# Kernel tuning notes

Hardware: AMD Instinct MI355X
Metric: run time of the kernel (lower is better)

Reference implementation:

```python
import jax, jax.numpy as jnp
import numpy as np

N = 10000      # num nodes
DEG = 8        # avg out-degree
E = N * DEG    # num bonds (directed edges)
D_IN = 128; D_HID = 128; D_OUT = 128; H = 16; HD = D_OUT // H
NG = 20; G_STOP = 10.0   # GaussianSmearing: 20 gaussians on [0, 10]
NF = 3                   # AngularEncoding num_funcs -> 1 + 4*NF = 13 feats


def _triplets(row, col, n):
    # numpy replica of BondUpdateLayer.triplets (SparseTensor version):
    # for each edge e=(j=row[e] -> i=col[e]), enumerate edges e'=(k -> j), drop k==i.
    order = np.argsort(col, kind='stable')          # edges sorted by target node
    in_count = np.bincount(col, minlength=n)
    in_start = np.concatenate([np.zeros(1, np.int64), np.cumsum(in_count)])
    num_t = in_count[row]                           # triplets per edge e
    T = int(num_t.sum())
    idx_ji = np.repeat(np.arange(row.size), num_t)
    within = np.arange(T) - np.repeat(np.cumsum(num_t) - num_t, num_t)
    idx_kj = order[in_start[row[idx_ji]] + within]
    idx_k = row[idx_kj]
    idx_i = col[idx_ji]
    idx_j = row[idx_ji]
    mask = idx_i != idx_k
    return idx_i[mask], idx_j[mask], idx_k[mask], idx_kj[mask], idx_ji[mask]


def setup_inputs() -> dict:
    key = jax.random.key(0)
    ks = jax.random.split(key, 8)
    rng = np.random.default_rng(0)
    src = np.repeat(np.arange(N), DEG)
    dst = (src + rng.integers(1, N, size=E)) % N    # random targets, never self-loop
    i_i, i_j, i_k, i_kj, i_ji = _triplets(src, dst, N)
    kv_dim = D_IN + 2 * NG + (1 + 4 * NF)           # 128 + 40 + 13 = 181

    def mlp_params(k, din):
        k1, k2 = jax.random.split(k)
        return {
            'W1': jax.random.normal(k1, (din, D_HID)) * 0.05, 'b1': jnp.zeros(D_HID),
            'g': jnp.ones(D_HID), 'b': jnp.zeros(D_HID),
            'W2': jax.random.normal(k2, (D_HID, D_OUT)) * 0.05, 'b2': jnp.zeros(D_OUT),
        }

    inp = {
        'h': jax.random.normal(ks[3], (N, D_IN)),
        'h_bond': jax.random.normal(ks[4], (E, D_IN)),
        'pos': jax.random.normal(ks[5], (N, 3)) * 3.0,
    }
    for name, k, din in (('hk', ks[0], kv_dim), ('hv', ks[1], kv_dim), ('hq', ks[2], D_IN)):
        for pn, v in mlp_params(k, din).items():
            inp[f'{name}_{pn}'] = v
    inp['bond_row'] = jnp.asarray(src, jnp.int32)
    inp['bond_col'] = jnp.asarray(dst, jnp.int32)
    inp['idx_i'] = jnp.asarray(i_i, jnp.int32)
    inp['idx_j'] = jnp.asarray(i_j, jnp.int32)
    inp['idx_k'] = jnp.asarray(i_k, jnp.int32)
    inp['idx_kj'] = jnp.asarray(i_kj, jnp.int32)
    inp['idx_ji'] = jnp.asarray(i_ji, jnp.int32)
    return inp


def _gauss(d):
    off = jnp.linspace(0.0, G_STOP, NG)
    coeff = -0.5 / (off[1] - off[0]) ** 2
    return jnp.exp(coeff * (d[:, None] - off) ** 2)


def _ang(a):
    freqs = jnp.asarray([1.0, 2.0, 3.0, 1.0, 0.5, 1.0 / 3.0])   # [i+1] + [1/(i+1)]
    x = a[:, None] * freqs
    return jnp.concatenate([a[:, None], jnp.sin(x), jnp.cos(x)], -1)


def _mlp(x, W1, b1, g, b, W2, b2):
    # Linear -> LayerNorm -> ReLU -> Linear
    hdn = x @ W1 + b1
    mu = hdn.mean(-1, keepdims=True)
    var = ((hdn - mu) ** 2).mean(-1, keepdims=True)
    hdn = jax.nn.relu(g * (hdn - mu) * jax.lax.rsqrt(var + 1e-5) + b)
    return hdn @ W2 + b2


def _forward(h, h_bond, pos,
             hk_W1, hk_b1, hk_g, hk_b, hk_W2, hk_b2,
             hv_W1, hv_b1, hv_g, hv_b, hv_W2, hv_b2,
             hq_W1, hq_b1, hq_g, hq_b, hq_W2, hq_b2,
             bond_row, bond_col, idx_i, idx_j, idx_k, idx_kj, idx_ji):
    # per-edge distance features (i=col, j=row in the torch code)
    dist = jnp.linalg.norm(pos[bond_col] - pos[bond_row], axis=-1)   # [E]
    r_feat = _gauss(dist)                                            # [E, 20]
    # per-triplet angle features
    pi = pos[idx_i]
    pji = pos[idx_j] - pi
    pki = pos[idx_k] - pi
    a = (pji * pki).sum(-1)
    bcr = jnp.linalg.norm(jnp.cross(pji, pki), axis=-1)
    a_feat = _ang(jnp.arctan2(bcr, a))                               # [T, 13]
    kv = jnp.concatenate([h_bond[idx_kj], r_feat[idx_kj], r_feat[idx_ji], a_feat], -1)  # [T, 181]
    T = kv.shape[0]
    k = _mlp(kv, hk_W1, hk_b1, hk_g, hk_b, hk_W2, hk_b2).reshape(T, H, HD)
    v = _mlp(kv, hv_W1, hv_b1, hv_g, hv_b, hv_W2, hv_b2).reshape(T, H, HD)
    q = _mlp(h_bond[idx_ji], hq_W1, hq_b1, hq_g, hq_b, hq_W2, hq_b2).reshape(T, H, HD)
    logits = (q * k).sum(-1) / np.sqrt(HD)                           # [T, H]
    # scatter_softmax over idx_ji (segments = edges)
    mx = jax.ops.segment_max(logits, idx_ji, num_segments=E)
    ex = jnp.exp(logits - mx[idx_ji])
    den = jax.ops.segment_sum(ex, idx_ji, num_segments=E)
    alpha = ex / den[idx_ji]                                         # [T, H]
    out = jax.ops.segment_sum(alpha[:, :, None] * v, idx_ji, num_segments=E)  # [E, H, HD]
    return out.reshape(E, D_OUT)


def reference(h, h_bond, pos,
              hk_W1, hk_b1, hk_g, hk_b, hk_W2, hk_b2,
              hv_W1, hv_b1, hv_g, hv_b, hv_W2, hv_b2,
              hq_W1, hq_b1, hq_g, hq_b, hq_W2, hq_b2,
              bond_row, bond_col, idx_i, idx_j, idx_k, idx_kj, idx_ji):
    return _forward(h, h_bond, pos,
                    hk_W1, hk_b1, hk_g, hk_b, hk_W2, hk_b2,
                    hv_W1, hv_b1, hv_g, hv_b, hv_W2, hv_b2,
                    hq_W1, hq_b1, hq_g, hq_b, hq_W2, hq_b2,
                    bond_row, bond_col, idx_i, idx_j, idx_k, idx_kj, idx_ji)
```

## Files before the change

kernel.cpp:

```cpp
#include <hip/hip_runtime.h>
#include <hip/hip_bf16.h>
#include <math.h>

typedef __hip_bfloat16 bf16;
typedef unsigned int u32;

__device__ __forceinline__ float b2f(bf16 x){ return __bfloat162float(x); }
__device__ __forceinline__ bf16  f2b(float x){ return __float2bfloat16(x); }
__device__ __forceinline__ float lo16(u32 u){ return __uint_as_float(u << 16); }
__device__ __forceinline__ float hi16(u32 u){ return __uint_as_float(u & 0xFFFF0000u); }
__device__ __forceinline__ u32 bfbits(float x){
    u32 u = __float_as_uint(x);
    return (u + 0x7FFFu + ((u >> 16) & 1u)) >> 16;
}

#define RSQRT8 0.35355339059327373f
#define G_STEP (10.0f/19.0f)
#define G_COEF (-0.5f/(G_STEP*G_STEP))

__device__ __forceinline__ constexpr int PERM4(int h){
    return ((h&1)<<3) | ((h&2)<<1) | ((h&4)>>1) | ((h&8)>>3);
}

__device__ __forceinline__ float fast_atan2(float y, float x){
    float ax = fabsf(x);
    float mn = fminf(y, ax), mx = fmaxf(y, ax);
    float t = mn / fmaxf(mx, 1e-30f);
    float s = t*t;
    float p = t * (0.99997726f + s*(-0.33262347f + s*(0.19354346f +
              s*(-0.11643287f + s*(0.05265332f + s*(-0.01172120f))))));
    float r = (y > ax) ? (1.5707963267948966f - p) : p;
    r = (x < 0.f) ? (3.14159265358979323f - r) : r;
    return r;
}


__global__ void seg_start_kernel(const int* __restrict__ idx_ji, int T,
                                 int* __restrict__ seg, int E)
{
    int e = blockIdx.x * blockDim.x + threadIdx.x;
    if (e > E) return;
    int lo = 0, hi = T;
    while (lo < hi) { int mid = (lo + hi) >> 1; if (idx_ji[mid] < e) lo = mid + 1; else hi = mid; }
    seg[e] = lo;
}

__global__ void marker_kernel(float* out, int n){
    int i = blockIdx.x * blockDim.x + threadIdx.x;
    if (i < n) out[i] = 12345.0f;
}

__global__ void pack_w2(const float* __restrict__ Wk2, const float* __restrict__ Wv2,
                        u32* __restrict__ kw2t, u32* __restrict__ vw2t)
{
    int idx = blockIdx.x*256 + threadIdx.x;
    if (idx >= 8192) return;
    int c = idx >> 6, p = idx & 63;
    kw2t[idx] = bfbits(Wk2[(size_t)(2*p)*128 + c]) | (bfbits(Wk2[(size_t)(2*p+1)*128 + c]) << 16);
    int j = idx >> 7, o = idx & 127;
    vw2t[idx] = bfbits(Wv2[(size_t)(2*j)*128 + o]) | (bfbits(Wv2[(size_t)(2*j+1)*128 + o]) << 16);
}

__global__ __launch_bounds__(128) void q_kernel(
    const float* __restrict__ W1, const float* __restrict__ B1,
    const float* __restrict__ G,  const float* __restrict__ Bln,
    const float* __restrict__ W2, const float* __restrict__ B2,
    const float* __restrict__ h_bond, bf16* __restrict__ qout, int E)
{
    __shared__ u32 sW[128*65];
    __shared__ float sH[16][130];
    __shared__ float sX[4][130];
    __shared__ float sRed[4][4];
    int tid = threadIdx.x; int wv = tid>>6, lane = tid&63;
    int base = blockIdx.x * 16;

    for (int idx = tid; idx < 128*128; idx += 128) {
        int i = idx >> 7, d = idx & 127;
        ((bf16*)sW)[d*130 + i] = f2b(W1[idx]);
    }
    __syncthreads();
    for (int e4 = 0; e4 < 16; e4 += 4) {
        #pragma unroll
        for (int q = 0; q < 4; ++q) {
            int e = base + e4 + q;
            sX[q][tid] = (e < E) ? h_bond[(size_t)e*128 + tid] : 0.f;
        }
        __syncthreads();
        float b1t = B1[tid];
        float ac[4] = {b1t, b1t, b1t, b1t};
        const u32* wrow = &sW[tid*65];
        #pragma unroll 4
        for (int j = 0; j < 64; ++j) {
            u32 w = wrow[j]; float wl = lo16(w), wh = hi16(w);
            #pragma unroll
            for (int q = 0; q < 4; ++q)
                ac[q] += sX[q][2*j]*wl + sX[q][2*j+1]*wh;
        }
        float s1v[4], s2v[4];
        #pragma unroll
        for (int q = 0; q < 4; ++q) { s1v[q] = ac[q]; s2v[q] = ac[q]*ac[q]; }
        #pragma unroll
        for (int m = 1; m < 64; m <<= 1) {
            #pragma unroll
            for (int q = 0; q < 4; ++q) {
                s1v[q] += __shfl_xor(s1v[q], m, 64);
                s2v[q] += __shfl_xor(s2v[q], m, 64);
            }
        }
        if (lane == 0) {
            #pragma unroll
            for (int q = 0; q < 4; ++q) { sRed[q][wv*2] = s1v[q]; sRed[q][wv*2+1] = s2v[q]; }
        }
        __syncthreads();
        float gt = G[tid], bt = Bln[tid];
        #pragma unroll
        for (int q = 0; q < 4; ++q) {
            float tot = sRed[q][0] + sRed[q][2], tot2 = sRed[q][1] + sRed[q][3];
            float mu = tot * (1.f/128.f);
            float var = fmaxf(tot2 * (1.f/128.f) - mu*mu, 0.f);
            float nv = gt * (ac[q] - mu) * rsqrtf(var + 1e-5f) + bt;
            sH[e4+q][tid] = fmaxf(nv, 0.f);
        }
        __syncthreads();
    }
    for (int idx = tid; idx < 128*128; idx += 128) {
        int i = idx >> 7, d = idx & 127;
        ((bf16*)sW)[d*130 + i] = f2b(W2[idx]);
    }
    __syncthreads();
    for (int e4 = 0; e4 < 16; e4 += 4) {
        float b2t = B2[tid];
        float ac[4] = {b2t, b2t, b2t, b2t};
        const u32* wrow = &sW[tid*65];
        #pragma unroll 4
        for (int j = 0; j < 64; ++j) {
            u32 w = wrow[j]; float wl = lo16(w), wh = hi16(w);
            #pragma unroll
            for (int q = 0; q < 4; ++q)
                ac[q] += sH[e4+q][2*j]*wl + sH[e4+q][2*j+1]*wh;
        }
        #pragma unroll
        for (int q = 0; q < 4; ++q) {
            int e = base + e4 + q;
            if (e < E) qout[(size_t)e*128 + tid] = f2b(ac[q]);
        }
    }
}

__global__ __launch_bounds__(128) void p_prep(
    const float* __restrict__ W1, const float* __restrict__ h_bond,
    const float* __restrict__ pos, const int* __restrict__ row,
    const int* __restrict__ col, bf16* __restrict__ P1, int E)
{
    __shared__ u32 sW[128*75];
    __shared__ float sX[4][152];
    int tid = threadIdx.x;
    for (int idx = tid; idx < 148*128; idx += 128) {
        int i = idx >> 7, d = idx & 127;
        ((bf16*)sW)[d*150 + i] = f2b(W1[idx]);
    }
    __syncthreads();
    int base = blockIdx.x * 16;
    for (int e4 = 0; e4 < 16; e4 += 4) {
        #pragma unroll
        for (int q = 0; q < 4; ++q) {
            int e = base + e4 + q;
            sX[q][tid] = (e < E) ? h_bond[(size_t)e*128 + tid] : 0.f;
        }
        if (tid < 80) {
            int q = tid / 20, g = tid % 20;
            int e = base + e4 + q;
            float rf = 0.f;
            if (e < E) {
                int i0 = col[e], j0 = row[e];
                float dx = pos[(size_t)i0*3+0] - pos[(size_t)j0*3+0];
                float dy = pos[(size_t)i0*3+1] - pos[(size_t)j0*3+1];
                float dz = pos[(size_t)i0*3+2] - pos[(size_t)j0*3+2];
                float dist = sqrtf(dx*dx + dy*dy + dz*dz);
                float t = dist - (float)g * G_STEP;
                rf = __expf(G_COEF * t * t);
            }
            sX[q][128 + g] = rf;
        }
        __syncthreads();
        float acc0 = 0.f, acc1 = 0.f, acc2 = 0.f, acc3 = 0.f;
        const u32* wrow = &sW[tid*75];
        #pragma unroll 4
        for (int j = 0; j < 74; ++j) {
            u32 w = wrow[j]; float wl = lo16(w), wh = hi16(w);
            acc0 += sX[0][2*j]*wl + sX[0][2*j+1]*wh;
            acc1 += sX[1][2*j]*wl + sX[1][2*j+1]*wh;
            acc2 += sX[2][2*j]*wl + sX[2][2*j+1]*wh;
            acc3 += sX[3][2*j]*wl + sX[3][2*j+1]*wh;
        }
        int e = base + e4;
        if (e   < E) P1[(size_t)e*128     + tid] = f2b(acc0);
        if (e+1 < E) P1[(size_t)(e+1)*128 + tid] = f2b(acc1);
        if (e+2 < E) P1[(size_t)(e+2)*128 + tid] = f2b(acc2);
        if (e+3 < E) P1[(size_t)(e+3)*128 + tid] = f2b(acc3);
        __syncthreads();
    }
}

#define EDGE_P2(W1full, b1v_, P2a_, P2b_) \
    float P2a_ = b1v_.x, P2b_ = b1v_.y; \
    { const float2* wbp = (const float2*)((W1full) + (size_t)148*128); \
      for (int g2 = 0; g2 < 20; ++g2) { \
        float tg = dist - (float)g2 * G_STEP; \
        float rf = __expf(G_COEF * tg * tg); \
        float2 wb = wbp[g2*64 + lane]; \
        P2a_ += rf * wb.x; \
        P2b_ += rf * wb.y; \
      } }

#define GEOM(S) \
    float dt##S = ax*bx##S + ay*by##S + az*bz##S; \
    float cxx##S = ay*bz##S - az*by##S, cyy##S = az*bx##S - ax*bz##S, czz##S = ax*by##S - ay*bx##S; \
    float bb##S = cxx##S*cxx##S + cyy##S*cyy##S + czz##S*czz##S; \
    float bc##S = sqrtf(bb##S); \
    float ih##S = rsqrtf(fmaxf(dt##S*dt##S + bb##S, 1e-30f)); \
    float c1##S = dt##S * ih##S, s1##S = bc##S * ih##S; \
    float ang##S = fast_atan2(bc##S, dt##S); \
    float sh##S = sqrtf(fmaxf(0.5f*(1.f - c1##S), 0.f)); \
    float ch##S = sqrtf(fmaxf(0.5f*(1.f + c1##S), 0.f)); \
    float st3##S, ct3##S; __sincosf((1.f/3.f)*ang##S, &st3##S, &ct3##S);

#define FEAT(fidx, valX, valY) { \
    u32 wk_ = sWA[0][(fidx)*64 + lane]; \
    u32 wu_ = sWA[1][(fidx)*64 + lane]; \
    float wkl_ = lo16(wk_), wkh_ = hi16(wk_), wvl_ = lo16(wu_), wvh_ = hi16(wu_); \
    float fx_ = (valX), fy_ = (valY); \
    v0kX += fx_*wkl_; v1kX += fx_*wkh_; v0vX += fx_*wvl_; v1vX += fx_*wvh_; \
    v0kY += fy_*wkl_; v1kY += fy_*wkh_; v0vY += fy_*wvl_; v1vY += fy_*wvh_; }

#define LNSTATS(v0_, v1_, TOT, TOT2) { \
    float sum_ = (v0_) + (v1_), ssq_ = (v0_)*(v0_) + (v1_)*(v1_); \
    float r_ = ((lane&1) ? ssq_ : sum_) + __shfl_xor((lane&1) ? sum_ : ssq_, 1, 64); \
    r_ += __shfl_xor(r_, 2, 64);  r_ += __shfl_xor(r_, 4, 64); \
    r_ += __shfl_xor(r_, 8, 64);  r_ += __shfl_xor(r_, 16, 64); \
    r_ += __shfl_xor(r_, 32, 64); \
    float o_ = __shfl_xor(r_, 1, 64); \
    TOT = (lane&1) ? o_ : r_;  TOT2 = (lane&1) ? r_ : o_; }

#define LNAPPLY(TOT, TOT2, v0_, v1_, g_, b_, H0, H1) { \
    float mu_ = (TOT) * (1.f/128.f); \
    float var_ = fmaxf((TOT2) * (1.f/128.f) - mu_*mu_, 0.f); \
    float rs_ = rsqrtf(var_ + 1e-5f); \
    H0 = fmaxf(g_.x*((v0_)-mu_)*rs_ + b_.x, 0.f); \
    H1 = fmaxf(g_.y*((v1_)-mu_)*rs_ + b_.y, 0.f); }

#define BFLY(P, LG) { \
    float a8_[8]; \
    { int up_ = lane & 1; \
      _Pragma("unroll") \
      for (int i_ = 0; i_ < 8; ++i_) { \
        float kp_ = up_ ? P[i_+8] : P[i_]; \
        float sd_ = up_ ? P[i_]   : P[i_+8]; \
        a8_[i_] = kp_ + __shfl_xor(sd_, 1, 64); } } \
    float a4_[4]; \
    { int up_ = lane & 2; \
      _Pragma("unroll") \
      for (int i_ = 0; i_ < 4; ++i_) { \
        float kp_ = up_ ? a8_[i_+4] : a8_[i_]; \
        float sd_ = up_ ? a8_[i_]   : a8_[i_+4]; \
        a4_[i_] = kp_ + __shfl_xor(sd_, 2, 64); } } \
    float a2_[2]; \
    { int up_ = lane & 4; \
      _Pragma("unroll") \
      for (int i_ = 0; i_ < 2; ++i_) { \
        float kp_ = up_ ? a4_[i_+2] : a4_[i_]; \
        float sd_ = up_ ? a4_[i_]   : a4_[i_+2]; \
        a2_[i_] = kp_ + __shfl_xor(sd_, 4, 64); } } \
    float a1_; \
    { int up_ = lane & 8; \
      float kp_ = up_ ? a2_[1] : a2_[0]; \
      float sd_ = up_ ? a2_[0] : a2_[1]; \
      a1_ = kp_ + __shfl_xor(sd_, 8, 64); } \
    a1_ += __shfl_xor(a1_, 16, 64); \
    a1_ += __shfl_xor(a1_, 32, 64); \
    LG = a1_ * RSQRT8; }

__global__ __launch_bounds__(256, 2)
void fused_kernel(
    const u32* __restrict__ kw2t, const u32* __restrict__ vw2t,
    const float* __restrict__ Wk1, const float* __restrict__ Bk1,
    const float* __restrict__ Gkg, const float* __restrict__ Bkln,
    const float* __restrict__ Wv1, const float* __restrict__ Bv1,
    const float* __restrict__ Gvg, const float* __restrict__ Bvln,
    const float* __restrict__ B2v,
    const bf16* __restrict__ qf, const bf16* __restrict__ P1k, const bf16* __restrict__ P1v,
    const float* __restrict__ pos, const int* __restrict__ seg,
    const int* __restrict__ idx_kj, const int* __restrict__ idx_k,
    const int* __restrict__ row, const int* __restrict__ col,
    float* __restrict__ out, int E)
{
    __shared__ u32 sS[4][16*66];
    __shared__ u32 sWA[2][11*64];
    __shared__ float2 sEx[4][16];
    int tid = threadIdx.x, lane = tid & 63, wv = tid >> 6;

    if (tid < 128) {
        int path = tid >> 6, l = tid & 63;
        const float* W1full = path ? Wv1 : Wk1;
        const float2* wap = (const float2*)(W1full + (size_t)168*128);
        float2 w0  = wap[ 0*64 + l];
        float2 w1  = wap[ 1*64 + l];
        float2 w2  = wap[ 2*64 + l];
        float2 w3  = wap[ 3*64 + l];
        float2 w4  = wap[ 4*64 + l];
        float2 w5  = wap[ 5*64 + l];
        float2 w6  = wap[ 6*64 + l];
        float2 w7  = wap[ 7*64 + l];
        float2 w8  = wap[ 8*64 + l];
        float2 w9  = wap[ 9*64 + l];
        float2 w10 = wap[10*64 + l];
        float2 w11 = wap[11*64 + l];
        float2 w12 = wap[12*64 + l];
        u32* dst = &sWA[path][0];
        dst[ 0*64 + l] = bfbits(w0.x)       | (bfbits(w0.y)       << 16);
        dst[ 1*64 + l] = bfbits(w1.x+w4.x)  | (bfbits(w1.y+w4.y)  << 16);
        dst[ 2*64 + l] = bfbits(w2.x)       | (bfbits(w2.y)       << 16);
        dst[ 3*64 + l] = bfbits(w3.x)       | (bfbits(w3.y)       << 16);
        dst[ 4*64 + l] = bfbits(w5.x)       | (bfbits(w5.y)       << 16);
        dst[ 5*64 + l] = bfbits(w6.x)       | (bfbits(w6.y)       << 16);
        dst[ 6*64 + l] = bfbits(w7.x+w10.x) | (bfbits(w7.y+w10.y) << 16);
        dst[ 7*64 + l] = bfbits(w8.x)       | (bfbits(w8.y)       << 16);
        dst[ 8*64 + l] = bfbits(w9.x)       | (bfbits(w9.y)       << 16);
        dst[ 9*64 + l] = bfbits(w11.x)      | (bfbits(w11.y)      << 16);
        dst[10*64 + l] = bfbits(w12.x)      | (bfbits(w12.y)      << 16);
    }
    __syncthreads();

    int e = __builtin_amdgcn_readfirstlane(blockIdx.x*4 + wv);
    if (e >= E) return;
    int s0 = __builtin_amdgcn_readfirstlane(seg[e]);
    int s1 = __builtin_amdgcn_readfirstlane(seg[e+1]);
    if (s1 <= s0) { out[(size_t)e*128 + lane] = 0.f; out[(size_t)e*128 + 64 + lane] = 0.f; return; }

    float2 b1k = ((const float2*)Bk1)[lane];
    float2 gk  = ((const float2*)Gkg)[lane];
    float2 bk  = ((const float2*)Bkln)[lane];
    float2 b1v = ((const float2*)Bv1)[lane];
    float2 gv  = ((const float2*)Gvg)[lane];
    float2 bv  = ((const float2*)Bvln)[lane];

    int i0 = __builtin_amdgcn_readfirstlane(col[e]);
    int j0 = __builtin_amdgcn_readfirstlane(row[e]);
    float pix = pos[(size_t)i0*3+0], piy = pos[(size_t)i0*3+1], piz = pos[(size_t)i0*3+2];
    float pjx = pos[(size_t)j0*3+0], pjy = pos[(size_t)j0*3+1], pjz = pos[(size_t)j0*3+2];
    float dxx = pix-pjx, dyy = piy-pjy, dzz = piz-pjz;
    float dist = sqrtf(dxx*dxx + dyy*dyy + dzz*dzz);

    EDGE_P2(Wk1, b1k, P2ak, P2bk);
    EDGE_P2(Wv1, b1v, P2av, P2bv);

    u32* sGkw = &sS[wv][0];
    {
        const u32* qrow = (const u32*)(qf + (size_t)e*128);
        #pragma unroll
        for (int h = 0; h < 16; ++h) {
            float g0 = 0.f, g1 = 0.f;
            #pragma unroll
            for (int j = 0; j < 4; ++j) {
                u32 qp = qrow[h*4 + j];
                float ql = lo16(qp), qh = hi16(qp);
                u32 w0 = kw2t[(h*8 + 2*j)*64 + lane];
                u32 w1 = kw2t[(h*8 + 2*j + 1)*64 + lane];
                g0 += ql*lo16(w0) + qh*lo16(w1);
                g1 += ql*hi16(w0) + qh*hi16(w1);
            }
            sGkw[h*64 + lane] = bfbits(g0) | (bfbits(g1) << 16);
        }
    }

    float S0[16], S1[16];
    #pragma unroll
    for (int h = 0; h < 16; ++h) { S0[h] = 0.f; S1[h] = 0.f; }
    float m = -1e30f, sden = 0.f;

    const u32* p1ku = (const u32*)P1k;
    const u32* p1vu = (const u32*)P1v;
    float ax = pjx-pix, ay = pjy-piy, az = pjz-piz;
    int perm = ((lane&1)<<3) | ((lane&2)<<1) | ((lane&4)>>1) | ((lane&8)>>3);

    int tB0 = (s0+1 < s1) ? s0+1 : s0;
    int kjX = __builtin_amdgcn_readfirstlane(idx_kj[s0]);
    int knX = __builtin_amdgcn_readfirstlane(idx_k[s0]);
    int kjY = __builtin_amdgcn_readfirstlane(idx_kj[tB0]);
    int knY = __builtin_amdgcn_readfirstlane(idx_k[tB0]);
    u32 fppkX = p1ku[(size_t)kjX*64 + lane], fppvX = p1vu[(size_t)kjX*64 + lane];
    u32 fppkY = p1ku[(size_t)kjY*64 + lane], fppvY = p1vu[(size_t)kjY*64 + lane];
    float fpkxX = pos[(size_t)knX*3+0], fpkyX = pos[(size_t)knX*3+1], fpkzX = pos[(size_t)knX*3+2];
    float fpkxY = pos[(size_t)knY*3+0], fpkyY = pos[(size_t)knY*3+1], fpkzY = pos[(size_t)knY*3+2];

    for (int t = s0; t < s1; t += 2) {
        const bool twoY = (t+1 < s1);
        u32 ppkX = fppkX, ppvX = fppvX, ppkY = fppkY, ppvY = fppvY;
        float bxX = fpkxX-pix, byX = fpkyX-piy, bzX = fpkzX-piz;
        float bxY = fpkxY-pix, byY = fpkyY-piy, bzY = fpkzY-piz;
        int tn0 = (t+2 < s1) ? t+2 : s1-1;
        int tn1 = (t+3 < s1) ? t+3 : s1-1;
        kjX = __builtin_amdgcn_readfirstlane(idx_kj[tn0]);
        knX = __builtin_amdgcn_readfirstlane(idx_k[tn0]);
        kjY = __builtin_amdgcn_readfirstlane(idx_kj[tn1]);
        knY = __builtin_amdgcn_readfirstlane(idx_k[tn1]);
        fppkX = p1ku[(size_t)kjX*64 + lane]; fppvX = p1vu[(size_t)kjX*64 + lane];
        fppkY = p1ku[(size_t)kjY*64 + lane]; fppvY = p1vu[(size_t)kjY*64 + lane];
        fpkxX = pos[(size_t)knX*3+0]; fpkyX = pos[(size_t)knX*3+1]; fpkzX = pos[(size_t)knX*3+2];
        fpkxY = pos[(size_t)knY*3+0]; fpkyY = pos[(size_t)knY*3+1]; fpkzY = pos[(size_t)knY*3+2];

        GEOM(X);
        GEOM(Y);

        float v0kX = P2ak + lo16(ppkX), v1kX = P2bk + hi16(ppkX);
        float v0vX = P2av + lo16(ppvX), v1vX = P2bv + hi16(ppvX);
        float v0kY = P2ak + lo16(ppkY), v1kY = P2bk + hi16(ppkY);
        float v0vY = P2av + lo16(ppvY), v1vY = P2bv + hi16(ppvY);

        FEAT(0,  angX, angY);
        FEAT(1,  s1X,  s1Y);
        FEAT(2,  2.f*s1X*c1X, 2.f*s1Y*c1Y);
        FEAT(3,  s1X*(3.f - 4.f*s1X*s1X), s1Y*(3.f - 4.f*s1Y*s1Y));
        FEAT(4,  shX,  shY);
        FEAT(5,  st3X, st3Y);
        FEAT(6,  c1X,  c1Y);
        FEAT(7,  1.f - 2.f*s1X*s1X, 1.f - 2.f*s1Y*s1Y);
        FEAT(8,  c1X*(4.f*c1X*c1X - 3.f), c1Y*(4.f*c1Y*c1Y - 3.f));
        FEAT(9,  chX,  chY);
        FEAT(10, ct3X, ct3Y);

        float totKX, tot2KX, totVX, tot2VX, totKY, tot2KY, totVY, tot2VY;
        LNSTATS(v0kX, v1kX, totKX, tot2KX);
        LNSTATS(v0vX, v1vX, totVX, tot2VX);
        LNSTATS(v0kY, v1kY, totKY, tot2KY);
        LNSTATS(v0vY, v1vY, totVY, tot2VY);
        float h0kX, h1kX, h0vX, h1vX, h0kY, h1kY, h0vY, h1vY;
        LNAPPLY(totKX, tot2KX, v0kX, v1kX, gk, bk, h0kX, h1kX);
        LNAPPLY(totVX, tot2VX, v0vX, v1vX, gv, bv, h0vX, h1vX);
        LNAPPLY(totKY, tot2KY, v0kY, v1kY, gk, bk, h0kY, h1kY);
        LNAPPLY(totVY, tot2VY, v0vY, v1vY, gv, bv, h0vY, h1vY);

        float pX[16], pY[16];
        #pragma unroll
        for (int h = 0; h < 16; ++h) {
            u32 g = sGkw[h*64 + lane];
            float gl = lo16(g), gh = hi16(g);
            pX[h] = h0kX*gl + h1kX*gh;
            pY[h] = h0kY*gl + h1kY*gh;
        }
        float lgX, lgY;
        BFLY(pX, lgX);
        BFLY(pY, lgY);

        float mx = fmaxf(lgX, lgY);
        if (__any(mx > m + 8.f)) {
            float nm = fmaxf(m, mx);
            float fac = __expf(m - nm);
            sden *= fac; m = nm;
            #pragma unroll
            for (int h = 0; h < 16; ++h) {
                float fh = __shfl(fac, PERM4(h), 64);
                S0[h] *= fh; S1[h] *= fh;
            }
        }
        float exX = __expf(lgX - m);
        float exY = twoY ? __expf(lgY - m) : 0.f;
        sden += exX + exY;
        if (lane < 16) sEx[wv][perm] = make_float2(exX, exY);
        #pragma unroll
        for (int h = 0; h < 16; ++h) {
            float2 eh = sEx[wv][h];
            S0[h] += eh.x*h0vX + eh.y*h0vY;
            S1[h] += eh.x*h1vX + eh.y*h1vY;
        }
    }

    float inv = 1.f / sden;
    #pragma unroll
    for (int h = 0; h < 16; ++h) {
        float sc = __shfl(inv, PERM4(h), 64);
        sS[wv][h*66 + lane] = bfbits(S0[h]*sc) | (bfbits(S1[h]*sc) << 16);
    }
    __threadfence_block();
    int h0i = lane >> 3, h1i = 8 + (lane >> 3);
    float acc0 = B2v[lane], acc1 = B2v[lane + 64];
    const u32* sr0 = &sS[wv][h0i*66];
    const u32* sr1 = &sS[wv][h1i*66];
    #pragma unroll 8
    for (int j = 0; j < 64; ++j) {
        u32 us0 = sr0[j], uw0 = vw2t[j*128 + lane];
        u32 us1 = sr1[j], uw1 = vw2t[j*128 + 64 + lane];
        acc0 += lo16(us0)*lo16(uw0) + hi16(us0)*hi16(uw0);
        acc1 += lo16(us1)*lo16(uw1) + hi16(us1)*hi16(uw1);
    }
    out[(size_t)e*128 + lane] = acc0;
    out[(size_t)e*128 + 64 + lane] = acc1;
}

extern "C" void kernel_launch(void* const* d_in, const int* in_sizes, int n_in,
                              void* d_out, int out_size, void* d_ws, size_t ws_size,
                              hipStream_t stream)
{
    const float* h_bond = (const float*)d_in[1];
    const float* pos    = (const float*)d_in[2];
    const float* hkW1 = (const float*)d_in[3];
    const float* hkb1 = (const float*)d_in[4];
    const float* hkg  = (const float*)d_in[5];
    const float* hkb  = (const float*)d_in[6];
    const float* hkW2 = (const float*)d_in[7];
    const float* hvW1 = (const float*)d_in[9];
    const float* hvb1 = (const float*)d_in[10];
    const float* hvg  = (const float*)d_in[11];
    const float* hvb  = (const float*)d_in[12];
    const float* hvW2 = (const float*)d_in[13];
    const float* hvb2 = (const float*)d_in[14];
    const float* hqW1 = (const float*)d_in[15];
    const float* hqb1 = (const float*)d_in[16];
    const float* hqg  = (const float*)d_in[17];
    const float* hqb  = (const float*)d_in[18];
    const float* hqW2 = (const float*)d_in[19];
    const float* hqb2 = (const float*)d_in[20];
    const int* row    = (const int*)d_in[21];
    const int* col    = (const int*)d_in[22];
    const int* idx_k  = (const int*)d_in[25];
    const int* idx_kj = (const int*)d_in[26];
    const int* idx_ji = (const int*)d_in[27];

    int E = in_sizes[21];
    int T = in_sizes[27];

    char* w = (char*)d_ws;
    size_t off = 0;
    auto carve = [&](size_t bytes) -> void* {
        void* p = w + off;
        off = (off + bytes + 255) & ~(size_t)255;
        return p;
    };
    int*  seg   = (int*) carve(((size_t)E + 1) * sizeof(int));
    bf16* qf    = (bf16*)carve((size_t)E * 128 * sizeof(bf16));
    bf16* P1k   = (bf16*)carve((size_t)E * 128 * sizeof(bf16));
    bf16* P1v   = (bf16*)carve((size_t)E * 128 * sizeof(bf16));
    u32*  kw2t  = (u32*) carve(8192 * sizeof(u32));
    u32*  vw2t  = (u32*) carve(8192 * sizeof(u32));

    if (off > ws_size) {
        marker_kernel<<<(out_size + 255)/256, 256, 0, stream>>>((float*)d_out, out_size);
        return;
    }

    int gq = (E + 15)/16;
    int gw = (E + 3)/4;
    seg_start_kernel<<<(E + 1 + 255)/256, 256, 0, stream>>>(idx_ji, T, seg, E);
    pack_w2<<<32, 256, 0, stream>>>(hkW2, hvW2, kw2t, vw2t);
    q_kernel<<<gq, 128, 0, stream>>>(hqW1, hqb1, hqg, hqb, hqW2, hqb2, h_bond, qf, E);
    p_prep<<<gq, 128, 0, stream>>>(hkW1, h_bond, pos, row, col, P1k, E);
    p_prep<<<gq, 128, 0, stream>>>(hvW1, h_bond, pos, row, col, P1v, E);
    fused_kernel<<<gw, 256, 0, stream>>>(kw2t, vw2t,
        hkW1, hkb1, hkg, hkb,
        hvW1, hvb1, hvg, hvb,
        hvb2, qf, P1k, P1v, pos, seg, idx_kj, idx_k, row, col, (float*)d_out, E);
}
```

Measured before the change: 1.628 ms.

## Make fused kernel persistent with atomic work-stealing over edges

```diff
diff --git a/kernel.cpp b/kernel.cpp
--- a/kernel.cpp
+++ b/kernel.cpp
@@ -36,9 +36,10 @@
 
 
 __global__ void seg_start_kernel(const int* __restrict__ idx_ji, int T,
-                                 int* __restrict__ seg, int E)
+                                 int* __restrict__ seg, int E, int* __restrict__ ctr)
 {
     int e = blockIdx.x * blockDim.x + threadIdx.x;
+    if (blockIdx.x == 0 && threadIdx.x == 0) *ctr = 0;
     if (e > E) return;
     int lo = 0, hi = T;
     while (lo < hi) { int mid = (lo + hi) >> 1; if (idx_ji[mid] < e) lo = mid + 1; else hi = mid; }
@@ -201,17 +202,6 @@
         __syncthreads();
     }
 }
-
-#define EDGE_P2(W1full, b1v_, P2a_, P2b_) \
-    float P2a_ = b1v_.x, P2b_ = b1v_.y; \
-    { const float2* wbp = (const float2*)((W1full) + (size_t)148*128); \
-      for (int g2 = 0; g2 < 20; ++g2) { \
-        float tg = dist - (float)g2 * G_STEP; \
-        float rf = __expf(G_COEF * tg * tg); \
-        float2 wb = wbp[g2*64 + lane]; \
-        P2a_ += rf * wb.x; \
-        P2b_ += rf * wb.y; \
-      } }
 
 #define GEOM(S) \
     float dt##S = ax*bx##S + ay*by##S + az*bz##S; \
@@ -292,7 +282,7 @@
     const float* __restrict__ pos, const int* __restrict__ seg,
     const int* __restrict__ idx_kj, const int* __restrict__ idx_k,
     const int* __restrict__ row, const int* __restrict__ col,
-    float* __restrict__ out, int E)
+    int* __restrict__ ctr, float* __restrict__ out, int E)
 {
     __shared__ u32 sS[4][16*66];
     __shared__ u32 sWA[2][11*64];
@@ -331,11 +321,9 @@
     }
     __syncthreads();
 
-    int e = __builtin_amdgcn_readfirstlane(blockIdx.x*4 + wv);
-    if (e >= E) return;
-    int s0 = __builtin_amdgcn_readfirstlane(seg[e]);
-    int s1 = __builtin_amdgcn_readfirstlane(seg[e+1]);
-    if (s1 <= s0) { out[(size_t)e*128 + lane] = 0.f; out[(size_t)e*128 + 64 + lane] = 0.f; return; }
+    int perm = ((lane&1)<<3) | ((lane&2)<<1) | ((lane&4)>>1) | ((lane&8)>>3);
+    const u32* p1ku = (const u32*)P1k;
+    const u32* p1vu = (const u32*)P1v;
 
     float2 b1k = ((const float2*)Bk1)[lane];
     float2 gk  = ((const float2*)Gkg)[lane];
@@ -344,157 +332,174 @@
     float2 gv  = ((const float2*)Gvg)[lane];
     float2 bv  = ((const float2*)Bvln)[lane];
 
-    int i0 = __builtin_amdgcn_readfirstlane(col[e]);
-    int j0 = __builtin_amdgcn_readfirstlane(row[e]);
-    float pix = pos[(size_t)i0*3+0], piy = pos[(size_t)i0*3+1], piz = pos[(size_t)i0*3+2];
-    float pjx = pos[(size_t)j0*3+0], pjy = pos[(size_t)j0*3+1], pjz = pos[(size_t)j0*3+2];
-    float dxx = pix-pjx, dyy = piy-pjy, dzz = piz-pjz;
-    float dist = sqrtf(dxx*dxx + dyy*dyy + dzz*dzz);
-
-    EDGE_P2(Wk1, b1k, P2ak, P2bk);
-    EDGE_P2(Wv1, b1v, P2av, P2bv);
-
-    u32* sGkw = &sS[wv][0];
-    {
-        const u32* qrow = (const u32*)(qf + (size_t)e*128);
+    for (;;) {
+        int e;
+        if (lane == 0) e = atomicAdd(ctr, 1);
+        e = __builtin_amdgcn_readfirstlane(__shfl(e, 0, 64));
+        if (e >= E) break;
+        int s0 = __builtin_amdgcn_readfirstlane(seg[e]);
+        int s1 = __builtin_amdgcn_readfirstlane(seg[e+1]);
+        if (s1 <= s0) { out[(size_t)e*128 + lane] = 0.f; out[(size_t)e*128 + 64 + lane] = 0.f; continue; }
+
+        int i0 = __builtin_amdgcn_readfirstlane(col[e]);
+        int j0 = __builtin_amdgcn_readfirstlane(row[e]);
+        float pix = pos[(size_t)i0*3+0], piy = pos[(size_t)i0*3+1], piz = pos[(size_t)i0*3+2];
+        float pjx = pos[(size_t)j0*3+0], pjy = pos[(size_t)j0*3+1], pjz = pos[(size_t)j0*3+2];
+        float dxx = pix-pjx, dyy = piy-pjy, dzz = piz-pjz;
+        float dist = sqrtf(dxx*dxx + dyy*dyy + dzz*dzz);
+
+        float P2ak = b1k.x, P2bk = b1k.y, P2av = b1v.x, P2bv = b1v.y;
+        {
+            const float2* wbk = (const float2*)(Wk1 + (size_t)148*128);
+            const float2* wbv = (const float2*)(Wv1 + (size_t)148*128);
+            for (int g2 = 0; g2 < 20; ++g2) {
+                float tg = dist - (float)g2 * G_STEP;
+                float rf = __expf(G_COEF * tg * tg);
+                float2 wk = wbk[g2*64 + lane];
+                float2 wu = wbv[g2*64 + lane];
+                P2ak += rf * wk.x; P2bk += rf * wk.y;
+                P2av += rf * wu.x; P2bv += rf * wu.y;
+            }
+        }
+
+        u32* sGkw = &sS[wv][0];
+        {
+            const u32* qrow = (const u32*)(qf + (size_t)e*128);
+            #pragma unroll
+            for (int h = 0; h < 16; ++h) {
+                float g0 = 0.f, g1 = 0.f;
+                #pragma unroll
+                for (int j = 0; j < 4; ++j) {
+                    u32 qp = qrow[h*4 + j];
+                    float ql = lo16(qp), qh = hi16(qp);
+                    u32 w0 = kw2t[(h*8 + 2*j)*64 + lane];
+                    u32 w1 = kw2t[(h*8 + 2*j + 1)*64 + lane];
+                    g0 += ql*lo16(w0) + qh*lo16(w1);
+                    g1 += ql*hi16(w0) + qh*hi16(w1);
+                }
+                sGkw[h*64 + lane] = bfbits(g0) | (bfbits(g1) << 16);
+            }
+        }
+
+        float S0[16], S1[16];
+        #pragma unroll
+        for (int h = 0; h < 16; ++h) { S0[h] = 0.f; S1[h] = 0.f; }
+        float m = -1e30f, sden = 0.f;
+        float ax = pjx-pix, ay = pjy-piy, az = pjz-piz;
+
+        int tB0 = (s0+1 < s1) ? s0+1 : s0;
+        int kjX = __builtin_amdgcn_readfirstlane(idx_kj[s0]);
+        int knX = __builtin_amdgcn_readfirstlane(idx_k[s0]);
+        int kjY = __builtin_amdgcn_readfirstlane(idx_kj[tB0]);
+        int knY = __builtin_amdgcn_readfirstlane(idx_k[tB0]);
+        u32 fppkX = p1ku[(size_t)kjX*64 + lane], fppvX = p1vu[(size_t)kjX*64 + lane];
+        u32 fppkY = p1ku[(size_t)kjY*64 + lane], fppvY = p1vu[(size_t)kjY*64 + lane];
+        float fpkxX = pos[(size_t)knX*3+0], fpkyX = pos[(size_t)knX*3+1], fpkzX = pos[(size_t)knX*3+2];
+        float fpkxY = pos[(size_t)knY*3+0], fpkyY = pos[(size_t)knY*3+1], fpkzY = pos[(size_t)knY*3+2];
+
+        for (int t = s0; t < s1; t += 2) {
+            const bool twoY = (t+1 < s1);
+            u32 ppkX = fppkX, ppvX = fppvX, ppkY = fppkY, ppvY = fppvY;
+            float bxX = fpkxX-pix, byX = fpkyX-piy, bzX = fpkzX-piz;
+            float bxY = fpkxY-pix, byY = fpkyY-piy, bzY = fpkzY-piz;
+            int tn0 = (t+2 < s1) ? t+2 : s1-1;
+            int tn1 = (t+3 < s1) ? t+3 : s1-1;
+            kjX = __builtin_amdgcn_readfirstlane(idx_kj[tn0]);
+            knX = __builtin_amdgcn_readfirstlane(idx_k[tn0]);
+            kjY = __builtin_amdgcn_readfirstlane(idx_kj[tn1]);
+            knY = __builtin_amdgcn_readfirstlane(idx_k[tn1]);
+            fppkX = p1ku[(size_t)kjX*64 + lane]; fppvX = p1vu[(size_t)kjX*64 + lane];
+            fppkY = p1ku[(size_t)kjY*64 + lane]; fppvY = p1vu[(size_t)kjY*64 + lane];
+            fpkxX = pos[(size_t)knX*3+0]; fpkyX = pos[(size_t)knX*3+1]; fpkzX = pos[(size_t)knX*3+2];
+            fpkxY = pos[(size_t)knY*3+0]; fpkyY = pos[(size_t)knY*3+1]; fpkzY = pos[(size_t)knY*3+2];
+
+            GEOM(X);
+            GEOM(Y);
+
+            float v0kX = P2ak + lo16(ppkX), v1kX = P2bk + hi16(ppkX);
+            float v0vX = P2av + lo16(ppvX), v1vX = P2bv + hi16(ppvX);
+            float v0kY = P2ak + lo16(ppkY), v1kY = P2bk + hi16(ppkY);
+            float v0vY = P2av + lo16(ppvY), v1vY = P2bv + hi16(ppvY);
+
+            FEAT(0,  angX, angY);
+            FEAT(1,  s1X,  s1Y);
+            FEAT(2,  2.f*s1X*c1X, 2.f*s1Y*c1Y);
+            FEAT(3,  s1X*(3.f - 4.f*s1X*s1X), s1Y*(3.f - 4.f*s1Y*s1Y));
+            FEAT(4,  shX,  shY);
+            FEAT(5,  st3X, st3Y);
+            FEAT(6,  c1X,  c1Y);
+            FEAT(7,  1.f - 2.f*s1X*s1X, 1.f - 2.f*s1Y*s1Y);
+            FEAT(8,  c1X*(4.f*c1X*c1X - 3.f), c1Y*(4.f*c1Y*c1Y - 3.f));
+            FEAT(9,  chX,  chY);
+            FEAT(10, ct3X, ct3Y);
+
+            float totKX, tot2KX, totVX, tot2VX, totKY, tot2KY, totVY, tot2VY;
+            LNSTATS(v0kX, v1kX, totKX, tot2KX);
+            LNSTATS(v0vX, v1vX, totVX, tot2VX);
+            LNSTATS(v0kY, v1kY, totKY, tot2KY);
+            LNSTATS(v0vY, v1vY, totVY, tot2VY);
+            float h0kX, h1kX, h0vX, h1vX, h0kY, h1kY, h0vY, h1vY;
+            LNAPPLY(totKX, tot2KX, v0kX, v1kX, gk, bk, h0kX, h1kX);
+            LNAPPLY(totVX, tot2VX, v0vX, v1vX, gv, bv, h0vX, h1vX);
+            LNAPPLY(totKY, tot2KY, v0kY, v1kY, gk, bk, h0kY, h1kY);
+            LNAPPLY(totVY, tot2VY, v0vY, v1vY, gv, bv, h0vY, h1vY);
+
+            float pX[16], pY[16];
+            #pragma unroll
+            for (int h = 0; h < 16; ++h) {
+                u32 g = sGkw[h*64 + lane];
+                float gl = lo16(g), gh = hi16(g);
+                pX[h] = h0kX*gl + h1kX*gh;
+                pY[h] = h0kY*gl + h1kY*gh;
+            }
+            float lgX, lgY;
+            BFLY(pX, lgX);
+            BFLY(pY, lgY);
+
+            float mx = fmaxf(lgX, lgY);
+            if (__any(mx > m + 8.f)) {
+                float nm = fmaxf(m, mx);
+                float fac = __expf(m - nm);
+                sden *= fac; m = nm;
+                #pragma unroll
+                for (int h = 0; h < 16; ++h) {
+                    float fh = __shfl(fac, PERM4(h), 64);
+                    S0[h] *= fh; S1[h] *= fh;
+                }
+            }
+            float exX = __expf(lgX - m);
+            float exY = twoY ? __expf(lgY - m) : 0.f;
+            sden += exX + exY;
+            if (lane < 16) sEx[wv][perm] = make_float2(exX, exY);
+            #pragma unroll
+            for (int h = 0; h < 16; ++h) {
+                float2 eh = sEx[wv][h];
+                S0[h] += eh.x*h0vX + eh.y*h0vY;
+                S1[h] += eh.x*h1vX + eh.y*h1vY;
+            }
+        }
+
+        float inv = 1.f / sden;
         #pragma unroll
         for (int h = 0; h < 16; ++h) {
-            float g0 = 0.f, g1 = 0.f;
-            #pragma unroll
-            for (int j = 0; j < 4; ++j) {
-                u32 qp = qrow[h*4 + j];
-                float ql = lo16(qp), qh = hi16(qp);
-                u32 w0 = kw2t[(h*8 + 2*j)*64 + lane];
-                u32 w1 = kw2t[(h*8 + 2*j + 1)*64 + lane];
-                g0 += ql*lo16(w0) + qh*lo16(w1);
-                g1 += ql*hi16(w0) + qh*hi16(w1);
-            }
-            sGkw[h*64 + lane] = bfbits(g0) | (bfbits(g1) << 16);
-        }
-    }
-
-    float S0[16], S1[16];
-    #pragma unroll
-    for (int h = 0; h < 16; ++h) { S0[h] = 0.f; S1[h] = 0.f; }
-    float m = -1e30f, sden = 0.f;
-
-    const u32* p1ku = (const u32*)P1k;
-    const u32* p1vu = (const u32*)P1v;
-    float ax = pjx-pix, ay = pjy-piy, az = pjz-piz;
-    int perm = ((lane&1)<<3) | ((lane&2)<<1) | ((lane&4)>>1) | ((lane&8)>>3);
-
-    int tB0 = (s0+1 < s1) ? s0+1 : s0;
-    int kjX = __builtin_amdgcn_readfirstlane(idx_kj[s0]);
-    int knX = __builtin_amdgcn_readfirstlane(idx_k[s0]);
-    int kjY = __builtin_amdgcn_readfirstlane(idx_kj[tB0]);
-    int knY = __builtin_amdgcn_readfirstlane(idx_k[tB0]);
-    u32 fppkX = p1ku[(size_t)kjX*64 + lane], fppvX = p1vu[(size_t)kjX*64 + lane];
-    u32 fppkY = p1ku[(size_t)kjY*64 + lane], fppvY = p1vu[(size_t)kjY*64 + lane];
-    float fpkxX = pos[(size_t)knX*3+0], fpkyX = pos[(size_t)knX*3+1], fpkzX = pos[(size_t)knX*3+2];
-    float fpkxY = pos[(size_t)knY*3+0], fpkyY = pos[(size_t)knY*3+1], fpkzY = pos[(size_t)knY*3+2];
-
-    for (int t = s0; t < s1; t += 2) {
-        const bool twoY = (t+1 < s1);
-        u32 ppkX = fppkX, ppvX = fppvX, ppkY = fppkY, ppvY = fppvY;
-        float bxX = fpkxX-pix, byX = fpkyX-piy, bzX = fpkzX-piz;
-        float bxY = fpkxY-pix, byY = fpkyY-piy, bzY = fpkzY-piz;
-        int tn0 = (t+2 < s1) ? t+2 : s1-1;
-        int tn1 = (t+3 < s1) ? t+3 : s1-1;
-        kjX = __builtin_amdgcn_readfirstlane(idx_kj[tn0]);
-        knX = __builtin_amdgcn_readfirstlane(idx_k[tn0]);
-        kjY = __builtin_amdgcn_readfirstlane(idx_kj[tn1]);
-        knY = __builtin_amdgcn_readfirstlane(idx_k[tn1]);
-        fppkX = p1ku[(size_t)kjX*64 + lane]; fppvX = p1vu[(size_t)kjX*64 + lane];
-        fppkY = p1ku[(size_t)kjY*64 + lane]; fppvY = p1vu[(size_t)kjY*64 + lane];
-        fpkxX = pos[(size_t)knX*3+0]; fpkyX = pos[(size_t)knX*3+1]; fpkzX = pos[(size_t)knX*3+2];
-        fpkxY = pos[(size_t)knY*3+0]; fpkyY = pos[(size_t)knY*3+1]; fpkzY = pos[(size_t)knY*3+2];
-
-        GEOM(X);
-        GEOM(Y);
-
-        float v0kX = P2ak + lo16(ppkX), v1kX = P2bk + hi16(ppkX);
-        float v0vX = P2av + lo16(ppvX), v1vX = P2bv + hi16(ppvX);
-        float v0kY = P2ak + lo16(ppkY), v1kY = P2bk + hi16(ppkY);
-        float v0vY = P2av + lo16(ppvY), v1vY = P2bv + hi16(ppvY);
-
-        FEAT(0,  angX, angY);
-        FEAT(1,  s1X,  s1Y);
-        FEAT(2,  2.f*s1X*c1X, 2.f*s1Y*c1Y);
-        FEAT(3,  s1X*(3.f - 4.f*s1X*s1X), s1Y*(3.f - 4.f*s1Y*s1Y));
-        FEAT(4,  shX,  shY);
-        FEAT(5,  st3X, st3Y);
-        FEAT(6,  c1X,  c1Y);
-        FEAT(7,  1.f - 2.f*s1X*s1X, 1.f - 2.f*s1Y*s1Y);
-        FEAT(8,  c1X*(4.f*c1X*c1X - 3.f), c1Y*(4.f*c1Y*c1Y - 3.f));
-        FEAT(9,  chX,  chY);
-        FEAT(10, ct3X, ct3Y);
-
-        float totKX, tot2KX, totVX, tot2VX, totKY, tot2KY, totVY, tot2VY;
-        LNSTATS(v0kX, v1kX, totKX, tot2KX);
-        LNSTATS(v0vX, v1vX, totVX, tot2VX);
-        LNSTATS(v0kY, v1kY, totKY, tot2KY);
-        LNSTATS(v0vY, v1vY, totVY, tot2VY);
-        float h0kX, h1kX, h0vX, h1vX, h0kY, h1kY, h0vY, h1vY;
-        LNAPPLY(totKX, tot2KX, v0kX, v1kX, gk, bk, h0kX, h1kX);
-        LNAPPLY(totVX, tot2VX, v0vX, v1vX, gv, bv, h0vX, h1vX);
-        LNAPPLY(totKY, tot2KY, v0kY, v1kY, gk, bk, h0kY, h1kY);
-        LNAPPLY(totVY, tot2VY, v0vY, v1vY, gv, bv, h0vY, h1vY);
-
-        float pX[16], pY[16];
-        #pragma unroll
-        for (int h = 0; h < 16; ++h) {
-            u32 g = sGkw[h*64 + lane];
-            float gl = lo16(g), gh = hi16(g);
-            pX[h] = h0kX*gl + h1kX*gh;
-            pY[h] = h0kY*gl + h1kY*gh;
-        }
-        float lgX, lgY;
-        BFLY(pX, lgX);
-        BFLY(pY, lgY);
-
-        float mx = fmaxf(lgX, lgY);
-        if (__any(mx > m + 8.f)) {
-            float nm = fmaxf(m, mx);
-            float fac = __expf(m - nm);
-            sden *= fac; m = nm;
-            #pragma unroll
-            for (int h = 0; h < 16; ++h) {
-                float fh = __shfl(fac, PERM4(h), 64);
-                S0[h] *= fh; S1[h] *= fh;
-            }
-        }
-        float exX = __expf(lgX - m);
-        float exY = twoY ? __expf(lgY - m) : 0.f;
-        sden += exX + exY;
-        if (lane < 16) sEx[wv][perm] = make_float2(exX, exY);
-        #pragma unroll
-        for (int h = 0; h < 16; ++h) {
-            float2 eh = sEx[wv][h];
-            S0[h] += eh.x*h0vX + eh.y*h0vY;
-            S1[h] += eh.x*h1vX + eh.y*h1vY;
-        }
-    }
-
-    float inv = 1.f / sden;
-    #pragma unroll
-    for (int h = 0; h < 16; ++h) {
-        float sc = __shfl(inv, PERM4(h), 64);
-        sS[wv][h*66 + lane] = bfbits(S0[h]*sc) | (bfbits(S1[h]*sc) << 16);
-    }
-    __threadfence_block();
-    int h0i = lane >> 3, h1i = 8 + (lane >> 3);
-    float acc0 = B2v[lane], acc1 = B2v[lane + 64];
-    const u32* sr0 = &sS[wv][h0i*66];
-    const u32* sr1 = &sS[wv][h1i*66];
-    #pragma unroll 8
-    for (int j = 0; j < 64; ++j) {
-        u32 us0 = sr0[j], uw0 = vw2t[j*128 + lane];
-        u32 us1 = sr1[j], uw1 = vw2t[j*128 + 64 + lane];
-        acc0 += lo16(us0)*lo16(uw0) + hi16(us0)*hi16(uw0);
-        acc1 += lo16(us1)*lo16(uw1) + hi16(us1)*hi16(uw1);
-    }
-    out[(size_t)e*128 + lane] = acc0;
-    out[(size_t)e*128 + 64 + lane] = acc1;
+            float sc = __shfl(inv, PERM4(h), 64);
+            sS[wv][h*66 + lane] = bfbits(S0[h]*sc) | (bfbits(S1[h]*sc) << 16);
+        }
+        __threadfence_block();
+        int h0i = lane >> 3, h1i = 8 + (lane >> 3);
+        float acc0 = B2v[lane], acc1 = B2v[lane + 64];
+        const u32* sr0 = &sS[wv][h0i*66];
+        const u32* sr1 = &sS[wv][h1i*66];
+        #pragma unroll 8
+        for (int j = 0; j < 64; ++j) {
+            u32 us0 = sr0[j], uw0 = vw2t[j*128 + lane];
+            u32 us1 = sr1[j], uw1 = vw2t[j*128 + 64 + lane];
+            acc0 += lo16(us0)*lo16(uw0) + hi16(us0)*hi16(uw0);
+            acc1 += lo16(us1)*lo16(uw1) + hi16(us1)*hi16(uw1);
+        }
+        out[(size_t)e*128 + lane] = acc0;
+        out[(size_t)e*128 + 64 + lane] = acc1;
+    }
 }
 
 extern "C" void kernel_launch(void* const* d_in, const int* in_sizes, int n_in,
@@ -542,6 +547,7 @@
     bf16* P1v   = (bf16*)carve((size_t)E * 128 * sizeof(bf16));
     u32*  kw2t  = (u32*) carve(8192 * sizeof(u32));
     u32*  vw2t  = (u32*) carve(8192 * sizeof(u32));
+    int*  ctr   = (int*) carve(256);
 
     if (off > ws_size) {
         marker_kernel<<<(out_size + 255)/256, 256, 0, stream>>>((float*)d_out, out_size);
@@ -549,14 +555,13 @@
     }
 
     int gq = (E + 15)/16;
-    int gw = (E + 3)/4;
-    seg_start_kernel<<<(E + 1 + 255)/256, 256, 0, stream>>>(idx_ji, T, seg, E);
+    seg_start_kernel<<<(E + 1 + 255)/256, 256, 0, stream>>>(idx_ji, T, seg, E, ctr);
     pack_w2<<<32, 256, 0, stream>>>(hkW2, hvW2, kw2t, vw2t);
     q_kernel<<<gq, 128, 0, stream>>>(hqW1, hqb1, hqg, hqb, hqW2, hqb2, h_bond, qf, E);
     p_prep<<<gq, 128, 0, stream>>>(hkW1, h_bond, pos, row, col, P1k, E);
     p_prep<<<gq, 128, 0, stream>>>(hvW1, h_bond, pos, row, col, P1v, E);
-    fused_kernel<<<gw, 256, 0, stream>>>(kw2t, vw2t,
+    fused_kernel<<<1024, 256, 0, stream>>>(kw2t, vw2t,
         hkW1, hkb1, hkg, hkb,
         hvW1, hvb1, hvg, hvb,
-        hvb2, qf, P1k, P1v, pos, seg, idx_kj, idx_k, row, col, (float*)d_out, E);
-}
+        hvb2, qf, P1k, P1v, pos, seg, idx_kj, idx_k, row, col, ctr, (float*)d_out, E);
+}
```

Result: slower. 4.003 ms (+145.8%).
